# Kernel tuning notes

Hardware: AMD Instinct MI355X
Metric: run time of the kernel (lower is better)

## Reference

```python
import jax, jax.numpy as jnp
import numpy as np


def _lap_mul(A, x):
    # L @ x with L = D^{-1/2} A D^{-1/2}, D = diag(rowsum(A))
    d = 1.0 / jnp.sqrt(jnp.sum(A, axis=-1))  # [N]
    return d[:, None] * (A @ (d[:, None] * x))


def setup_inputs() -> dict:
    key = jax.random.key(0)
    k1, k2, k3, k4, k5, k6 = jax.random.split(key, 6)
    N, D_IN, D_OUT = 4096, 128, 128
    x = jax.random.normal(k1, (N, D_IN), dtype=jnp.float32)
    A = jax.random.uniform(k2, (N, N), dtype=jnp.float32)
    # linear params stored as [in, out] (apply via x @ W + b)
    s1 = 1.0 / np.sqrt(D_IN)
    W1 = jax.random.uniform(k3, (D_IN, D_OUT), minval=-s1, maxval=s1, dtype=jnp.float32)
    b1 = jax.random.uniform(k4, (D_OUT,), minval=-s1, maxval=s1, dtype=jnp.float32)
    W2 = jax.random.uniform(k5, (D_IN, D_OUT), minval=-s1, maxval=s1, dtype=jnp.float32)
    b2 = jax.random.uniform(k6, (D_OUT,), minval=-s1, maxval=s1, dtype=jnp.float32)
    return {"x": x, "A": A, "W1": W1, "b1": b1, "W2": W2, "b2": b2, "sigma": 1, "k": 4}


def reference(x, A, W1, b1, W2, b2, sigma, k):
    # first graph conv + linear1 + leaky relu
    z = _lap_mul(A, x) @ W1 + b1            # [N, d_out]
    z = jax.nn.leaky_relu(z, negative_slope=0.1)

    # pairwise Euclidean distance (efficient cdist form, same math as the
    # original broadcasted (z_i - z_j)**2 sum, without the d x N x N blowup)
    sq = jnp.sum(z * z, axis=-1)            # [N]
    d2 = sq[:, None] + sq[None, :] - 2.0 * (z @ z.T)
    d2 = jnp.maximum(d2, 0.0)
    S = jnp.sqrt(d2 + 1e-10)                # [N, N]
    S = jnp.exp(-S / (2.0 * sigma))

    # double-argsort rank -> keep top-k per row (emulates original masking)
    order = jnp.argsort(-S, axis=-1)
    ranks = jnp.argsort(order, axis=-1)
    S = jnp.where(ranks < k, S, 0.0)

    A2 = S + A
    out = _lap_mul(A2, x) @ W2 + b2         # [N, d_out]
    return out
```

## Files before the change

### kernel.cpp

```cpp
#include <hip/hip_runtime.h>
#include <cstdint>
#include <cstddef>

#define NN 4096
#define DD 128

using short8 = __attribute__((ext_vector_type(8))) short;
using f32x4  = __attribute__((ext_vector_type(4))) float;
typedef unsigned long long u64;

typedef __attribute__((address_space(1))) void gvoid;
typedef __attribute__((address_space(3))) void lvoid;

__device__ __forceinline__ void async16(const void* g, void* l) {
  __builtin_amdgcn_global_load_lds((gvoid*)g, (lvoid*)l, 16, 0, 0);
}

__device__ __forceinline__ float dec_f(const void* p) {
  if (!p) return 1.0f;
  int b = *(const int*)p;
  return (b >= 0 && b < 1000000) ? (float)b : __int_as_float(b);
}
__device__ __forceinline__ int dec_i(const void* p) {
  if (!p) return 4;
  int b = *(const int*)p;
  return (b >= 0 && b < 1000000) ? b : (int)__int_as_float(b);
}

__device__ __forceinline__ unsigned short f2bf(float f) {
  union { float f; unsigned int u; } v; v.f = f;
  unsigned int u = v.u;
  unsigned int r = (u + 0x7fffu + ((u >> 16) & 1u)) >> 16;
  return (unsigned short)r;
}

__device__ __forceinline__ void ins4(u64 (&l)[4], u64 k) {
#pragma unroll
  for (int t = 0; t < 4; ++t) {
    u64 old = l[t];
    bool bt = k < old;
    l[t] = bt ? k : old;
    k = bt ? old : k;
  }
}

template <int ROWS, int KC, int NTHR>
__device__ __forceinline__ void stage2(const unsigned short* src, int row0, int kb,
                                       unsigned short* dst, int tid, int stride) {
  const int CPR = KC / 8;
  const int ITER = (ROWS * CPR) / NTHR;
#pragma unroll
  for (int t = 0; t < ITER; ++t) {
    int id = tid + t * NTHR;
    int r = id / CPR;
    int p = id % CPR;
    int lc = p ^ (r & 7);
    const void* g = src + (size_t)(row0 + r) * stride + kb + lc * 8;
    async16(g, dst + (size_t)(id & ~63) * 8);
  }
}

template <int CPR>
__device__ __forceinline__ short8 fragN(const unsigned short* t, int row, int ch) {
  return *(const short8*)(t + (size_t)(row * CPR + (ch ^ (row & 7))) * 8);
}

__global__ __launch_bounds__(256) void k_rowsum_scale(
    const float* __restrict__ A, const float* __restrict__ x,
    float* __restrict__ rowsumA, float* __restrict__ dvec, float* __restrict__ V,
    unsigned short* __restrict__ Ah) {
  int row = blockIdx.x;
  int tid = threadIdx.x;
  const float4* Arow = (const float4*)(A + (size_t)row * NN);
  float s = 0.f;
#pragma unroll
  for (int l = 0; l < 4; ++l) {
    int idx = tid + l * 256;
    float4 v = Arow[idx];
    s += (v.x + v.y) + (v.z + v.w);
    ushort4 h = {f2bf(v.x), f2bf(v.y), f2bf(v.z), f2bf(v.w)};
    *(ushort4*)(Ah + (size_t)row * NN + idx * 4) = h;
  }
  __shared__ float red[256];
  __shared__ float dsh;
  red[tid] = s;
  __syncthreads();
  if (tid < 64) {
    s = red[tid] + red[tid + 64] + red[tid + 128] + red[tid + 192];
#pragma unroll
    for (int off = 32; off > 0; off >>= 1) s += __shfl_down(s, off, 64);
    if (tid == 0) { rowsumA[row] = s; float d = rsqrtf(s); dvec[row] = d; dsh = d; }
  }
  __syncthreads();
  float d = dsh;
  if (tid < 32) {
    float4 xv = ((const float4*)(x + (size_t)row * DD))[tid];
    float4 o; o.x = d * xv.x; o.y = d * xv.y; o.z = d * xv.z; o.w = d * xv.w;
    ((float4*)(V + (size_t)row * DD))[tid] = o;
  }
}

__global__ __launch_bounds__(256) void k_xw(
    const float* __restrict__ X, const float* __restrict__ W, float* __restrict__ P) {
  int r0 = blockIdx.x * 16;
  int tid = threadIdx.x;
  int tr = tid >> 4, tc = tid & 15;
  __shared__ float Xs[16 * 132];
  __shared__ float Ws[32 * 128];
#pragma unroll
  for (int l = 0; l < 8; ++l) {
    int idx = tid + l * 256;
    int r = idx >> 7, c = idx & 127;
    Xs[r * 132 + c] = X[(size_t)(r0 + r) * DD + c];
  }
  float acc[8];
#pragma unroll
  for (int u = 0; u < 8; ++u) acc[u] = 0.f;
  for (int t0 = 0; t0 < 128; t0 += 32) {
    __syncthreads();
#pragma unroll
    for (int l = 0; l < 4; ++l) {
      int idx = tid + l * 256;
      int tt = idx >> 5, c4 = (idx & 31) << 2;
      *(float4*)(Ws + tt * 128 + c4) = *(const float4*)(W + (size_t)(t0 + tt) * DD + c4);
    }
    __syncthreads();
#pragma unroll 8
    for (int tt = 0; tt < 32; ++tt) {
      float g = Xs[tr * 132 + t0 + tt];
      float4 w0 = *(const float4*)(Ws + tt * 128 + tc * 8);
      float4 w1 = *(const float4*)(Ws + tt * 128 + tc * 8 + 4);
      acc[0] = fmaf(g, w0.x, acc[0]); acc[1] = fmaf(g, w0.y, acc[1]);
      acc[2] = fmaf(g, w0.z, acc[2]); acc[3] = fmaf(g, w0.w, acc[3]);
      acc[4] = fmaf(g, w1.x, acc[4]); acc[5] = fmaf(g, w1.y, acc[5]);
      acc[6] = fmaf(g, w1.z, acc[6]); acc[7] = fmaf(g, w1.w, acc[7]);
    }
  }
  size_t off = (size_t)(r0 + tr) * DD + tc * 8;
  float4 o0 = {acc[0], acc[1], acc[2], acc[3]};
  float4 o1 = {acc[4], acc[5], acc[6], acc[7]};
  *(float4*)(P + off) = o0;
  *(float4*)(P + off + 4) = o1;
}

__global__ __launch_bounds__(256) void k_vt(
    const float* __restrict__ U, unsigned short* __restrict__ UTh) {
  __shared__ float Ls[64 * 132];
  int bx = blockIdx.x, tid = threadIdx.x;
  int r0 = bx * 64;
#pragma unroll
  for (int l = 0; l < 8; ++l) {
    int idx = tid + l * 256;
    int r = idx >> 5, c4 = (idx & 31) << 2;
    *(float4*)(Ls + r * 132 + c4) = *(const float4*)(U + (size_t)(r0 + r) * DD + c4);
  }
  __syncthreads();
  int c = tid >> 1, rh = tid & 1;
  unsigned short hb[32];
#pragma unroll
  for (int i = 0; i < 32; ++i) hb[i] = f2bf(Ls[(rh * 32 + i) * 132 + c]);
  size_t base = (size_t)c * NN + r0 + rh * 32;
#pragma unroll
  for (int q = 0; q < 8; ++q) {
    ushort4 h = {hb[q * 4], hb[q * 4 + 1], hb[q * 4 + 2], hb[q * 4 + 3]};
    *(ushort4*)(UTh + base + q * 4) = h;
  }
}

template <int SPLIT>
__global__ __launch_bounds__(256) void k_gemm_bf16(
    const unsigned short* __restrict__ Ah, const unsigned short* __restrict__ Bh,
    float* __restrict__ G) {
  __shared__ __align__(16) unsigned short As_h[128 * 64];
  __shared__ __align__(16) unsigned short Bs_h[128 * 64];

  int bx = blockIdx.x;
  int mt = bx / SPLIT, sp = bx % SPLIT;
  int m0 = mt * 128;
  const int KLEN = NN / SPLIT;
  int ks = sp * KLEN;
  int tid = threadIdx.x, lane = tid & 63, w = tid >> 6;
  int wm = w >> 1, wn = w & 1;
  int l15 = lane & 15, quad = lane >> 4;

  f32x4 acc[4][4];
#pragma unroll
  for (int a = 0; a < 4; ++a)
#pragma unroll
    for (int b = 0; b < 4; ++b) acc[a][b] = (f32x4){0.f, 0.f, 0.f, 0.f};

  for (int kt = 0; kt < KLEN; kt += 64) {
    int kb = ks + kt;
    __syncthreads();
    stage2<128, 64, 256>(Ah, m0, kb, As_h, tid, NN);
    stage2<128, 64, 256>(Bh, 0, kb, Bs_h, tid, NN);
    __syncthreads();
#pragma unroll
    for (int k0 = 0; k0 < 64; k0 += 32) {
      int ch = (k0 >> 3) + quad;
      short8 a_h[4], b_h[4];
#pragma unroll
      for (int f = 0; f < 4; ++f) {
        a_h[f] = fragN<8>(As_h, wm * 64 + f * 16 + l15, ch);
        b_h[f] = fragN<8>(Bs_h, wn * 64 + f * 16 + l15, ch);
      }
#pragma unroll
      for (int fm = 0; fm < 4; ++fm)
#pragma unroll
        for (int fn = 0; fn < 4; ++fn)
          acc[fm][fn] = __builtin_amdgcn_mfma_f32_16x16x32_bf16(a_h[fm], b_h[fn], acc[fm][fn], 0, 0, 0);
    }
  }
  float* Gp = G + (size_t)sp * NN * DD;
#pragma unroll
  for (int fm = 0; fm < 4; ++fm) {
    int rb = m0 + wm * 64 + fm * 16 + quad * 4;
#pragma unroll
    for (int fn = 0; fn < 4; ++fn) {
      int c = wn * 64 + fn * 16 + l15;
#pragma unroll
      for (int i = 0; i < 4; ++i)
        Gp[(size_t)(rb + i) * DD + c] = acc[fm][fn][i];
    }
  }
}

template <int NP>
__global__ __launch_bounds__(256) void k_red(
    const float* __restrict__ G, const float* __restrict__ dvec,
    const float* __restrict__ bvec, int leaky,
    float* __restrict__ Out, unsigned short* __restrict__ zh,
    float* __restrict__ sqout,
    const float* __restrict__ Usp, const float* __restrict__ sval,
    const int* __restrict__ sidx, const void* kptr) {
  int r0 = blockIdx.x * 16;
  int tid = threadIdx.x;
  int tr = tid >> 4, tc = tid & 15;
  int r = r0 + tr;
  size_t off = (size_t)r * DD + tc * 8;
  __shared__ float red[256];

  float acc[8];
#pragma unroll
  for (int u = 0; u < 8; ++u) acc[u] = 0.f;
#pragma unroll
  for (int p = 0; p < NP; ++p) {
    const float* gp = G + (size_t)p * NN * DD + off;
    float4 g0 = *(const float4*)gp;
    float4 g1 = *(const float4*)(gp + 4);
    acc[0] += g0.x; acc[1] += g0.y; acc[2] += g0.z; acc[3] += g0.w;
    acc[4] += g1.x; acc[5] += g1.y; acc[6] += g1.z; acc[7] += g1.w;
  }
  if (sidx != nullptr) {
    int kk = dec_i(kptr); kk = kk < 1 ? 1 : (kk > 4 ? 4 : kk);
    for (int t = 0; t < kk; ++t) {
      float sv = sval[r * 8 + t];
      int id = sidx[r * 8 + t];
      const float* vr = Usp + (size_t)id * DD + tc * 8;
      float4 w0 = *(const float4*)vr;
      float4 w1 = *(const float4*)(vr + 4);
      acc[0] = fmaf(sv, w0.x, acc[0]); acc[1] = fmaf(sv, w0.y, acc[1]);
      acc[2] = fmaf(sv, w0.z, acc[2]); acc[3] = fmaf(sv, w0.w, acc[3]);
      acc[4] = fmaf(sv, w1.x, acc[4]); acc[5] = fmaf(sv, w1.y, acc[5]);
      acc[6] = fmaf(sv, w1.z, acc[6]); acc[7] = fmaf(sv, w1.w, acc[7]);
    }
  }
  float d = dvec[r];
  float4 b0 = *(const float4*)(bvec + tc * 8);
  float4 b1 = *(const float4*)(bvec + tc * 8 + 4);
  float bb[8] = {b0.x, b0.y, b0.z, b0.w, b1.x, b1.y, b1.z, b1.w};
  float o[8];
#pragma unroll
  for (int u = 0; u < 8; ++u) {
    float v = fmaf(d, acc[u], bb[u]);
    if (leaky) v = v > 0.f ? v : 0.1f * v;
    o[u] = v;
  }
  if (Out) {
    float4 o0 = {o[0], o[1], o[2], o[3]};
    float4 o1 = {o[4], o[5], o[6], o[7]};
    *(float4*)(Out + off) = o0;
    *(float4*)(Out + off + 4) = o1;
  }
  if (zh) {
    ushort4 h0 = {f2bf(o[0]), f2bf(o[1]), f2bf(o[2]), f2bf(o[3])};
    ushort4 h1 = {f2bf(o[4]), f2bf(o[5]), f2bf(o[6]), f2bf(o[7])};
    *(ushort4*)(zh + off) = h0;
    *(ushort4*)(zh + off + 4) = h1;
  }
  if (sqout != nullptr) {
    float p = 0.f;
#pragma unroll
    for (int u = 0; u < 8; ++u) p = fmaf(o[u], o[u], p);
    red[tid] = p;
    __syncthreads();
    if (tc == 0) {
      float s = 0.f;
#pragma unroll
      for (int i = 0; i < 16; ++i) s += red[tr * 16 + i];
      sqout[r] = s;
    }
  }
}

__global__ __launch_bounds__(512, 8) void k_scores(
    const unsigned short* __restrict__ Zh,
    const float* __restrict__ sq, u64* __restrict__ pkey) {
  __shared__ __align__(16) unsigned short Am[64 * 128];
  __shared__ __align__(16) unsigned short Bj[64 * 128];
  float* Stile = (float*)&Bj[0];
  u64* mv = (u64*)&Am[0];

  int bx = blockIdx.x;
  int mt = bx >> 4, jp = bx & 15;
  int m0 = mt * 64, j0 = jp * 256;
  int tid = threadIdx.x, lane = tid & 63, w = tid >> 6;
  int wm = w >> 2, wn = w & 3;
  int l15 = lane & 15, quad = lane >> 4;

  stage2<64, 128, 512>(Zh, m0, 0, Am, tid, DD);

  int srow = tid >> 3;
  int sc = tid & 7;
  float sqi_r = sq[m0 + srow];

  u64 lst[4];
#pragma unroll
  for (int s = 0; s < 4; ++s) lst[s] = ~0ull;

  for (int jt = 0; jt < 4; ++jt) {
    int jrow0 = j0 + jt * 64;
    __syncthreads();
    stage2<64, 128, 512>(Zh, jrow0, 0, Bj, tid, DD);
    __syncthreads();

    f32x4 acc[2];
    acc[0] = (f32x4){0.f, 0.f, 0.f, 0.f};
    acc[1] = (f32x4){0.f, 0.f, 0.f, 0.f};
#pragma unroll
    for (int kc = 0; kc < 4; ++kc) {
      int ch = kc * 4 + quad;
      short8 ah0 = fragN<16>(Am, wm * 32 + l15, ch);
      short8 ah1 = fragN<16>(Am, wm * 32 + 16 + l15, ch);
      short8 bh  = fragN<16>(Bj, wn * 16 + l15, ch);
      acc[0] = __builtin_amdgcn_mfma_f32_16x16x32_bf16(ah0, bh, acc[0], 0, 0, 0);
      acc[1] = __builtin_amdgcn_mfma_f32_16x16x32_bf16(ah1, bh, acc[1], 0, 0, 0);
    }
    __syncthreads();

    {
      int c = wn * 16 + l15;
      float sqjv = sq[jrow0 + c];
      int cslot = c >> 2, cw = c & 3;
#pragma unroll
      for (int fm = 0; fm < 2; ++fm) {
        int rb = wm * 32 + fm * 16 + quad * 4;
#pragma unroll
        for (int i = 0; i < 4; ++i) {
          int r = rb + i;
          Stile[r * 64 + ((cslot ^ (r & 7)) << 2) + cw] = fmaf(-2.f, acc[fm][i], sqjv);
        }
      }
    }
    __syncthreads();

#pragma unroll
    for (int q = 0; q < 2; ++q) {
      int slot = sc * 2 + q;
      float4 kv = *(const float4*)(Stile + srow * 64 + ((slot ^ (srow & 7)) << 2));
      int jb = jrow0 + sc * 8 + q * 4;
      float ke[4] = {kv.x, kv.y, kv.z, kv.w};
#pragma unroll
      for (int e = 0; e < 4; ++e) {
        float v = fmaxf(sqi_r + ke[e], 0.f);
        ins4(lst, ((u64)__float_as_uint(v) << 32) | (unsigned)(jb + e));
      }
    }
  }

  __syncthreads();
#pragma unroll
  for (int s = 0; s < 4; ++s) mv[tid * 4 + s] = lst[s];
  __syncthreads();
  if (tid < 64) {
    u64 best[4] = {~0ull, ~0ull, ~0ull, ~0ull};
    for (int g = 0; g < 8; ++g) {
      int src = tid * 8 + g;
#pragma unroll
      for (int s = 0; s < 4; ++s) ins4(best, mv[src * 4 + s]);
    }
#pragma unroll
    for (int s = 0; s < 4; ++s)
      pkey[((size_t)(m0 + tid) * 16 + jp) * 4 + s] = best[s];
  }
}

__global__ __launch_bounds__(256) void k_merge(
    const u64* __restrict__ pkey,
    const float* __restrict__ rowsumA, const float* __restrict__ x,
    float* __restrict__ sval, int* __restrict__ sidx,
    float* __restrict__ d2vec, float* __restrict__ V,
    const void* kptr, const void* sigptr) {
  int bx = blockIdx.x;
  int r0 = bx * 16;
  int tid = threadIdx.x;
  int kk = dec_i(kptr); kk = kk < 1 ? 1 : (kk > 4 ? 4 : kk);
  float inv2s = 0.5f / dec_f(sigptr);
  __shared__ float ds[16];
  if (tid < 16) {
    int r = r0 + tid;
    u64 best[4] = {~0ull, ~0ull, ~0ull, ~0ull};
    for (int p = 0; p < 16; ++p) {
#pragma unroll
      for (int s = 0; s < 4; ++s) ins4(best, pkey[((size_t)r * 16 + p) * 4 + s]);
    }
    float srw = 0.f;
#pragma unroll
    for (int s = 0; s < 4; ++s) {
      if (s < kk) {
        float d2 = __uint_as_float((unsigned)(best[s] >> 32));
        float S = __expf(-sqrtf(d2 + 1e-10f) * inv2s);
        sval[r * 8 + s] = S;
        sidx[r * 8 + s] = (int)(best[s] & 0xffffffffu);
        srw += S;
      }
    }
    float dd = rsqrtf(rowsumA[r] + srw);
    d2vec[r] = dd;
    ds[tid] = dd;
  }
  __syncthreads();
#pragma unroll
  for (int l = 0; l < 2; ++l) {
    int idx = tid + l * 256;
    int rl = idx >> 5;
    int c4 = (idx & 31) << 2;
    float4 xv = *(const float4*)(x + (size_t)(r0 + rl) * DD + c4);
    float dd = ds[rl];
    float4 o; o.x = dd * xv.x; o.y = dd * xv.y; o.z = dd * xv.z; o.w = dd * xv.w;
    *(float4*)(V + (size_t)(r0 + rl) * DD + c4) = o;
  }
}

extern "C" void kernel_launch(void* const* d_in, const int* in_sizes, int n_in,
                              void* d_out, int out_size, void* d_ws, size_t ws_size,
                              hipStream_t stream) {
  const float* x  = (const float*)d_in[0];
  const float* A  = (const float*)d_in[1];
  const float* W1 = (const float*)d_in[2];
  const float* b1 = (const float*)d_in[3];
  const float* W2 = (const float*)d_in[4];
  const float* b2 = (const float*)d_in[5];
  const void* sig = (n_in > 6) ? d_in[6] : nullptr;
  const void* kp  = (n_in > 7) ? d_in[7] : nullptr;

  float* ws = (float*)d_ws;
  float* rowsumA = ws;
  float* dvec    = ws + 4096;
  float* d2vec   = ws + 8192;
  float* sqv     = ws + 12288;
  float* sval    = ws + 16384;
  int*   sidx    = (int*)(ws + 49152);
  u64*   pkey    = (u64*)(ws + 81920);
  unsigned short* Zh = (unsigned short*)(ws + 606208);
  float* V       = ws + 868352;
  float* U       = ws + 1392640;
  unsigned short* UTh = (unsigned short*)(ws + 1916928);
  unsigned short* Ah  = (unsigned short*)(ws + 2179072);
  float* G       = ws + 10567680;

  const size_t F16 = 10567680 + 16 * 524288;
  int split16 = (ws_size >= F16 * 4);

  k_rowsum_scale<<<4096, 256, 0, stream>>>(A, x, rowsumA, dvec, V, Ah);
  k_xw<<<256, 256, 0, stream>>>(V, W1, U);
  k_vt<<<64, 256, 0, stream>>>(U, UTh);
  if (split16) {
    k_gemm_bf16<16><<<512, 256, 0, stream>>>(Ah, UTh, G);
    k_red<16><<<256, 256, 0, stream>>>(G, dvec, b1, 1, nullptr, Zh, sqv,
                                       nullptr, nullptr, nullptr, nullptr);
  } else {
    k_gemm_bf16<4><<<128, 256, 0, stream>>>(Ah, UTh, G);
    k_red<4><<<256, 256, 0, stream>>>(G, dvec, b1, 1, nullptr, Zh, sqv,
                                      nullptr, nullptr, nullptr, nullptr);
  }
  k_scores<<<1024, 512, 0, stream>>>(Zh, sqv, pkey);
  k_merge<<<256, 256, 0, stream>>>(pkey, rowsumA, x, sval, sidx, d2vec, V, kp, sig);
  k_xw<<<256, 256, 0, stream>>>(V, W2, U);
  k_vt<<<64, 256, 0, stream>>>(U, UTh);
  if (split16) {
    k_gemm_bf16<16><<<512, 256, 0, stream>>>(Ah, UTh, G);
    k_red<16><<<256, 256, 0, stream>>>(G, d2vec, b2, 0, (float*)d_out, nullptr, nullptr,
                                       U, sval, sidx, kp);
  } else {
    k_gemm_bf16<4><<<128, 256, 0, stream>>>(Ah, UTh, G);
    k_red<4><<<256, 256, 0, stream>>>(G, d2vec, b2, 0, (float*)d_out, nullptr, nullptr,
                                      U, sval, sidx, kp);
  }
}
```

Measured before the change: 209.7 us.

## Fuse row scaling, X·W, merge and bf16 transpose into one kernel

The separate V-scaling, x@W, transpose-to-bf16 and top-k merge kernels are combined into a templated k_xwt kernel that scales x by the degree vector in shared memory, multiplies by W, and writes the transposed bf16 result directly. This removes several launches and the global round trips through V and U (U is still written in mode 2 because the final reduction uses it). In exchange the fused kernel runs on only 64 blocks of 64 rows each, so parallelism drops and the merge step is serialized ahead of the GEMM within each block.

Result: no change. 210.7 us (+0.5%).

```diff
diff --git a/kernel.cpp b/kernel.cpp
--- a/kernel.cpp
+++ b/kernel.cpp
@@ -66,8 +66,8 @@
 }
 
 __global__ __launch_bounds__(256) void k_rowsum_scale(
-    const float* __restrict__ A, const float* __restrict__ x,
-    float* __restrict__ rowsumA, float* __restrict__ dvec, float* __restrict__ V,
+    const float* __restrict__ A,
+    float* __restrict__ rowsumA, float* __restrict__ dvec,
     unsigned short* __restrict__ Ah) {
   int row = blockIdx.x;
   int tid = threadIdx.x;
@@ -82,40 +82,78 @@
     *(ushort4*)(Ah + (size_t)row * NN + idx * 4) = h;
   }
   __shared__ float red[256];
-  __shared__ float dsh;
   red[tid] = s;
   __syncthreads();
   if (tid < 64) {
     s = red[tid] + red[tid + 64] + red[tid + 128] + red[tid + 192];
 #pragma unroll
     for (int off = 32; off > 0; off >>= 1) s += __shfl_down(s, off, 64);
-    if (tid == 0) { rowsumA[row] = s; float d = rsqrtf(s); dvec[row] = d; dsh = d; }
-  }
-  __syncthreads();
-  float d = dsh;
-  if (tid < 32) {
-    float4 xv = ((const float4*)(x + (size_t)row * DD))[tid];
-    float4 o; o.x = d * xv.x; o.y = d * xv.y; o.z = d * xv.z; o.w = d * xv.w;
-    ((float4*)(V + (size_t)row * DD))[tid] = o;
-  }
-}
-
-__global__ __launch_bounds__(256) void k_xw(
-    const float* __restrict__ X, const float* __restrict__ W, float* __restrict__ P) {
-  int r0 = blockIdx.x * 16;
-  int tid = threadIdx.x;
-  int tr = tid >> 4, tc = tid & 15;
-  __shared__ float Xs[16 * 132];
+    if (tid == 0) { rowsumA[row] = s; dvec[row] = rsqrtf(s); }
+  }
+}
+
+template <int MODE>
+__global__ __launch_bounds__(256) void k_xwt(
+    const float* __restrict__ x, const float* __restrict__ W,
+    const float* __restrict__ dsrc,
+    const u64* __restrict__ pkey, const float* __restrict__ rowsumA,
+    float* __restrict__ sval, int* __restrict__ sidx, float* __restrict__ d2vec,
+    float* __restrict__ Uout, unsigned short* __restrict__ UTh,
+    const void* kptr, const void* sigptr) {
+  __shared__ float Vs[64 * 132];
   __shared__ float Ws[32 * 128];
+  __shared__ float dsm[64];
+  int bx = blockIdx.x, tid = threadIdx.x;
+  int r0 = bx * 64;
+
+  if (MODE == 1) {
+    if (tid < 64) dsm[tid] = dsrc[r0 + tid];
+  } else {
+    if (tid < 64) {
+      int r = r0 + tid;
+      u64 best[4] = {~0ull, ~0ull, ~0ull, ~0ull};
+      for (int p = 0; p < 16; ++p) {
+#pragma unroll
+        for (int s = 0; s < 4; ++s) ins4(best, pkey[((size_t)r * 16 + p) * 4 + s]);
+      }
+      int kk = dec_i(kptr); kk = kk < 1 ? 1 : (kk > 4 ? 4 : kk);
+      float inv2s = 0.5f / dec_f(sigptr);
+      float srw = 0.f;
+#pragma unroll
+      for (int s = 0; s < 4; ++s) {
+        if (s < kk) {
+          float d2 = __uint_as_float((unsigned)(best[s] >> 32));
+          float S = __expf(-sqrtf(d2 + 1e-10f) * inv2s);
+          sval[r * 8 + s] = S;
+          sidx[r * 8 + s] = (int)(best[s] & 0xffffffffu);
+          srw += S;
+        }
+      }
+      float dd = rsqrtf(rowsumA[r] + srw);
+      d2vec[r] = dd;
+      dsm[tid] = dd;
+    }
+  }
+  __syncthreads();
 #pragma unroll
   for (int l = 0; l < 8; ++l) {
     int idx = tid + l * 256;
-    int r = idx >> 7, c = idx & 127;
-    Xs[r * 132 + c] = X[(size_t)(r0 + r) * DD + c];
-  }
-  float acc[8];
-#pragma unroll
-  for (int u = 0; u < 8; ++u) acc[u] = 0.f;
+    int r = idx >> 5, c4 = (idx & 31) << 2;
+    float4 xv = *(const float4*)(x + (size_t)(r0 + r) * DD + c4);
+    float dd = dsm[r];
+    Vs[r * 132 + c4 + 0] = dd * xv.x;
+    Vs[r * 132 + c4 + 1] = dd * xv.y;
+    Vs[r * 132 + c4 + 2] = dd * xv.z;
+    Vs[r * 132 + c4 + 3] = dd * xv.w;
+  }
+
+  int tr = tid >> 4, tc = tid & 15;
+  float acc[4][8];
+#pragma unroll
+  for (int rr = 0; rr < 4; ++rr)
+#pragma unroll
+    for (int u = 0; u < 8; ++u) acc[rr][u] = 0.f;
+
   for (int t0 = 0; t0 < 128; t0 += 32) {
     __syncthreads();
 #pragma unroll
@@ -127,43 +165,47 @@
     __syncthreads();
 #pragma unroll 8
     for (int tt = 0; tt < 32; ++tt) {
-      float g = Xs[tr * 132 + t0 + tt];
       float4 w0 = *(const float4*)(Ws + tt * 128 + tc * 8);
       float4 w1 = *(const float4*)(Ws + tt * 128 + tc * 8 + 4);
-      acc[0] = fmaf(g, w0.x, acc[0]); acc[1] = fmaf(g, w0.y, acc[1]);
-      acc[2] = fmaf(g, w0.z, acc[2]); acc[3] = fmaf(g, w0.w, acc[3]);
-      acc[4] = fmaf(g, w1.x, acc[4]); acc[5] = fmaf(g, w1.y, acc[5]);
-      acc[6] = fmaf(g, w1.z, acc[6]); acc[7] = fmaf(g, w1.w, acc[7]);
-    }
-  }
-  size_t off = (size_t)(r0 + tr) * DD + tc * 8;
-  float4 o0 = {acc[0], acc[1], acc[2], acc[3]};
-  float4 o1 = {acc[4], acc[5], acc[6], acc[7]};
-  *(float4*)(P + off) = o0;
-  *(float4*)(P + off + 4) = o1;
-}
-
-__global__ __launch_bounds__(256) void k_vt(
-    const float* __restrict__ U, unsigned short* __restrict__ UTh) {
-  __shared__ float Ls[64 * 132];
-  int bx = blockIdx.x, tid = threadIdx.x;
-  int r0 = bx * 64;
-#pragma unroll
-  for (int l = 0; l < 8; ++l) {
-    int idx = tid + l * 256;
-    int r = idx >> 5, c4 = (idx & 31) << 2;
-    *(float4*)(Ls + r * 132 + c4) = *(const float4*)(U + (size_t)(r0 + r) * DD + c4);
-  }
-  __syncthreads();
-  int c = tid >> 1, rh = tid & 1;
-  unsigned short hb[32];
-#pragma unroll
-  for (int i = 0; i < 32; ++i) hb[i] = f2bf(Ls[(rh * 32 + i) * 132 + c]);
-  size_t base = (size_t)c * NN + r0 + rh * 32;
-#pragma unroll
-  for (int q = 0; q < 8; ++q) {
-    ushort4 h = {hb[q * 4], hb[q * 4 + 1], hb[q * 4 + 2], hb[q * 4 + 3]};
-    *(ushort4*)(UTh + base + q * 4) = h;
+#pragma unroll
+      for (int rr = 0; rr < 4; ++rr) {
+        float g = Vs[(tr * 4 + rr) * 132 + t0 + tt];
+        acc[rr][0] = fmaf(g, w0.x, acc[rr][0]); acc[rr][1] = fmaf(g, w0.y, acc[rr][1]);
+        acc[rr][2] = fmaf(g, w0.z, acc[rr][2]); acc[rr][3] = fmaf(g, w0.w, acc[rr][3]);
+        acc[rr][4] = fmaf(g, w1.x, acc[rr][4]); acc[rr][5] = fmaf(g, w1.y, acc[rr][5]);
+        acc[rr][6] = fmaf(g, w1.z, acc[rr][6]); acc[rr][7] = fmaf(g, w1.w, acc[rr][7]);
+      }
+    }
+  }
+
+  if (MODE == 2) {
+#pragma unroll
+    for (int rr = 0; rr < 4; ++rr) {
+      size_t off = (size_t)(r0 + tr * 4 + rr) * DD + tc * 8;
+      float4 o0 = {acc[rr][0], acc[rr][1], acc[rr][2], acc[rr][3]};
+      float4 o1 = {acc[rr][4], acc[rr][5], acc[rr][6], acc[rr][7]};
+      *(float4*)(Uout + off) = o0;
+      *(float4*)(Uout + off + 4) = o1;
+    }
+  }
+  __syncthreads();
+#pragma unroll
+  for (int rr = 0; rr < 4; ++rr)
+#pragma unroll
+    for (int cc = 0; cc < 8; ++cc)
+      Vs[(tc * 8 + cc) * 64 + tr * 4 + rr] = acc[rr][cc];
+  __syncthreads();
+  {
+    int c = tid >> 1, h = tid & 1;
+    unsigned short hb[32];
+#pragma unroll
+    for (int i = 0; i < 32; ++i) hb[i] = f2bf(Vs[c * 64 + h * 32 + i]);
+    size_t base = (size_t)c * NN + r0 + h * 32;
+#pragma unroll
+    for (int q = 0; q < 8; ++q) {
+      ushort4 hh = {hb[q * 4], hb[q * 4 + 1], hb[q * 4 + 2], hb[q * 4 + 3]};
+      *(ushort4*)(UTh + base + q * 4) = hh;
+    }
   }
 }
 
@@ -395,53 +437,6 @@
   }
 }
 
-__global__ __launch_bounds__(256) void k_merge(
-    const u64* __restrict__ pkey,
-    const float* __restrict__ rowsumA, const float* __restrict__ x,
-    float* __restrict__ sval, int* __restrict__ sidx,
-    float* __restrict__ d2vec, float* __restrict__ V,
-    const void* kptr, const void* sigptr) {
-  int bx = blockIdx.x;
-  int r0 = bx * 16;
-  int tid = threadIdx.x;
-  int kk = dec_i(kptr); kk = kk < 1 ? 1 : (kk > 4 ? 4 : kk);
-  float inv2s = 0.5f / dec_f(sigptr);
-  __shared__ float ds[16];
-  if (tid < 16) {
-    int r = r0 + tid;
-    u64 best[4] = {~0ull, ~0ull, ~0ull, ~0ull};
-    for (int p = 0; p < 16; ++p) {
-#pragma unroll
-      for (int s = 0; s < 4; ++s) ins4(best, pkey[((size_t)r * 16 + p) * 4 + s]);
-    }
-    float srw = 0.f;
-#pragma unroll
-    for (int s = 0; s < 4; ++s) {
-      if (s < kk) {
-        float d2 = __uint_as_float((unsigned)(best[s] >> 32));
-        float S = __expf(-sqrtf(d2 + 1e-10f) * inv2s);
-        sval[r * 8 + s] = S;
-        sidx[r * 8 + s] = (int)(best[s] & 0xffffffffu);
-        srw += S;
-      }
-    }
-    float dd = rsqrtf(rowsumA[r] + srw);
-    d2vec[r] = dd;
-    ds[tid] = dd;
-  }
-  __syncthreads();
-#pragma unroll
-  for (int l = 0; l < 2; ++l) {
-    int idx = tid + l * 256;
-    int rl = idx >> 5;
-    int c4 = (idx & 31) << 2;
-    float4 xv = *(const float4*)(x + (size_t)(r0 + rl) * DD + c4);
-    float dd = ds[rl];
-    float4 o; o.x = dd * xv.x; o.y = dd * xv.y; o.z = dd * xv.z; o.w = dd * xv.w;
-    *(float4*)(V + (size_t)(r0 + rl) * DD + c4) = o;
-  }
-}
-
 extern "C" void kernel_launch(void* const* d_in, const int* in_sizes, int n_in,
                               void* d_out, int out_size, void* d_ws, size_t ws_size,
                               hipStream_t stream) {
@@ -463,7 +458,6 @@
   int*   sidx    = (int*)(ws + 49152);
   u64*   pkey    = (u64*)(ws + 81920);
   unsigned short* Zh = (unsigned short*)(ws + 606208);
-  float* V       = ws + 868352;
   float* U       = ws + 1392640;
   unsigned short* UTh = (unsigned short*)(ws + 1916928);
   unsigned short* Ah  = (unsigned short*)(ws + 2179072);
@@ -472,9 +466,10 @@
   const size_t F16 = 10567680 + 16 * 524288;
   int split16 = (ws_size >= F16 * 4);
 
-  k_rowsum_scale<<<4096, 256, 0, stream>>>(A, x, rowsumA, dvec, V, Ah);
-  k_xw<<<256, 256, 0, stream>>>(V, W1, U);
-  k_vt<<<64, 256, 0, stream>>>(U, UTh);
+  k_rowsum_scale<<<4096, 256, 0, stream>>>(A, rowsumA, dvec, Ah);
+  k_xwt<1><<<64, 256, 0, stream>>>(x, W1, dvec, nullptr, nullptr,
+                                   nullptr, nullptr, nullptr, nullptr, UTh,
+                                   nullptr, nullptr);
   if (split16) {
     k_gemm_bf16<16><<<512, 256, 0, stream>>>(Ah, UTh, G);
     k_red<16><<<256, 256, 0, stream>>>(G, dvec, b1, 1, nullptr, Zh, sqv,
@@ -485,9 +480,8 @@
                                       nullptr, nullptr, nullptr, nullptr);
   }
   k_scores<<<1024, 512, 0, stream>>>(Zh, sqv, pkey);
-  k_merge<<<256, 256, 0, stream>>>(pkey, rowsumA, x, sval, sidx, d2vec, V, kp, sig);
-  k_xw<<<256, 256, 0, stream>>>(V, W2, U);
-  k_vt<<<64, 256, 0, stream>>>(U, UTh);
+  k_xwt<2><<<64, 256, 0, stream>>>(x, W2, nullptr, pkey, rowsumA,
+                                   sval, sidx, d2vec, U, UTh, kp, sig);
   if (split16) {
     k_gemm_bf16<16><<<512, 256, 0, stream>>>(Ah, UTh, G);
     k_red<16><<<256, 256, 0, stream>>>(G, d2vec, b2, 0, (float*)d_out, nullptr, nullptr,
```
